# Kernel optimization log

Measured on AMD Instinct MI355X. Metric: run time of the kernel, lower is better.

Reference implementation:

```python
import jax, jax.numpy as jnp
import numpy as np

B = 4
T, Hh, Ww = 16, 32, 32
C = 256
HEADS = 8
WIN = 4
SHIFT = 2
MLP = 1024


def _rel_pos_index(w):
    coords = np.stack(np.meshgrid(np.arange(w), np.arange(w), np.arange(w), indexing='ij')).reshape(3, -1)
    rc = (coords[:, :, None] - coords[:, None, :]).transpose(1, 2, 0)
    rc[:, :, 0] += w - 1
    rc[:, :, 1] += w - 1
    rc[:, :, 2] += w - 1
    rc[:, :, 0] *= (2 * w - 1) * (2 * w - 1)
    rc[:, :, 1] *= 2 * w - 1
    return rc.sum(-1).astype(np.int32)  # (w^3, w^3)


def _attn_mask(t, h, w, win, shift):
    m = np.zeros((t, h, w))
    sl = (slice(0, -win), slice(-win, -shift), slice(-shift, None))
    cnt = 0
    for a in sl:
        for b in sl:
            for c in sl:
                m[a, b, c] = cnt
                cnt += 1
    m = m.reshape(t // win, win, h // win, win, w // win, win).transpose(0, 2, 4, 1, 3, 5).reshape(-1, win ** 3)
    am = m[:, None, :] - m[:, :, None]  # (nW, N, N)
    return np.where(am != 0, -100.0, 0.0).astype(np.float32)


def setup_inputs() -> dict:
    key = jax.random.key(0)
    ks = jax.random.split(key, 12)
    s_in = 1.0 / np.sqrt(C)
    s_mlp = 1.0 / np.sqrt(MLP)
    return {
        'x': jax.random.normal(ks[0], (B, T * Hh * Ww, C), jnp.float32),
        'norm1_g': jnp.ones((C,), jnp.float32),
        'norm1_b': jnp.zeros((C,), jnp.float32),
        'qkv_w': jax.random.normal(ks[1], (C, 3 * C), jnp.float32) * s_in,
        'qkv_b': jax.random.normal(ks[2], (3 * C,), jnp.float32) * 0.02,
        'proj_w': jax.random.normal(ks[3], (C, C), jnp.float32) * s_in,
        'proj_b': jax.random.normal(ks[4], (C,), jnp.float32) * 0.02,
        'rel_bias_table': jax.random.normal(ks[5], ((2 * WIN - 1) ** 3, HEADS), jnp.float32) * 0.02,
        'norm2_g': jnp.ones((C,), jnp.float32),
        'norm2_b': jnp.zeros((C,), jnp.float32),
        'mlp_w1': jax.random.normal(ks[6], (C, MLP), jnp.float32) * s_in,
        'mlp_b1': jax.random.normal(ks[7], (MLP,), jnp.float32) * 0.02,
        'mlp_w2': jax.random.normal(ks[8], (MLP, C), jnp.float32) * s_mlp,
        'mlp_b2': jax.random.normal(ks[9], (C,), jnp.float32) * 0.02,
        'rel_index': jnp.asarray(_rel_pos_index(WIN)),
        'attn_mask': jnp.asarray(_attn_mask(T, Hh, Ww, WIN, SHIFT)),
    }


def _ln(x, g, b, eps):
    mu = x.mean(-1, keepdims=True)
    var = ((x - mu) ** 2).mean(-1, keepdims=True)
    return (x - mu) * jax.lax.rsqrt(var + eps) * g + b


def reference(x, norm1_g, norm1_b, qkv_w, qkv_b, proj_w, proj_b, rel_bias_table,
              norm2_g, norm2_b, mlp_w1, mlp_b1, mlp_w2, mlp_b2, rel_index, attn_mask):
    w = WIN
    N = w ** 3
    hd = C // HEADS
    scale = hd ** -0.5

    h = _ln(x, norm1_g, norm1_b, 1e-5).reshape(B, T, Hh, Ww, C)
    h = jnp.roll(h, shift=(-SHIFT, -SHIFT, -SHIFT), axis=(1, 2, 3))
    # window partition -> (B*nW, N, C)
    h = h.reshape(B, T // w, w, Hh // w, w, Ww // w, w, C)
    h = h.transpose(0, 1, 3, 5, 2, 4, 6, 7).reshape(-1, N, C)

    qkv = (h @ qkv_w + qkv_b).reshape(-1, N, 3, HEADS, hd)
    qkv = qkv.transpose(2, 0, 3, 1, 4)  # (3, BW, heads, N, hd)
    q, k, v = qkv[0] * scale, qkv[1], qkv[2]
    attn = jnp.einsum('bhid,bhjd->bhij', q, k)

    bias = rel_bias_table[rel_index.reshape(-1)].reshape(N, N, HEADS).transpose(2, 0, 1)
    attn = attn + bias[None]

    nW = attn_mask.shape[0]
    attn = attn.reshape(-1, nW, HEADS, N, N) + attn_mask[None, :, None]
    attn = jax.nn.softmax(attn.reshape(-1, HEADS, N, N), axis=-1)

    o = jnp.einsum('bhij,bhjd->bhid', attn, v).transpose(0, 2, 1, 3).reshape(-1, N, C)
    o = o @ proj_w + proj_b
    # window reverse
    o = o.reshape(B, T // w, Hh // w, Ww // w, w, w, w, C)
    o = o.transpose(0, 1, 4, 2, 5, 3, 6, 7).reshape(B, T, Hh, Ww, C)
    o = jnp.roll(o, shift=(SHIFT, SHIFT, SHIFT), axis=(1, 2, 3)).reshape(B, T * Hh * Ww, C)

    x = x + o
    y = _ln(x, norm2_g, norm2_b, 1e-6)
    y = jax.nn.gelu(y @ mlp_w1 + mlp_b1, approximate=False) @ mlp_w2 + mlp_b2
    return x + y
```

## Files before the change

### kernel.cpp

```cpp
#include <hip/hip_runtime.h>
#include <cstdint>
#include <cstddef>

typedef float  f32x4_t  __attribute__((ext_vector_type(4)));
typedef __bf16 bf16x8_t __attribute__((ext_vector_type(8)));
typedef __bf16 bf16x4_t __attribute__((ext_vector_type(4)));

#define NTOK   65536
#define CCH    256
#define NWINT  1024

__device__ __forceinline__ float wred_sum(float v) {
#pragma unroll
  for (int off = 32; off > 0; off >>= 1) v += __shfl_xor(v, off, 64);
  return v;
}

__device__ __forceinline__ void gload16(void* lds, const void* g) {
  __builtin_amdgcn_global_load_lds(
      (const __attribute__((address_space(1))) uint32_t*)g,
      (__attribute__((address_space(3))) uint32_t*)lds, 16, 0, 0);
}

__device__ __forceinline__ int win_to_orig(int token) {
  int gid = token >> 6, n = token & 63;
  int bb = gid >> 8, rem = gid & 255;
  int t = (((rem >> 6) << 2) + (n >> 4) + 2) & 15;
  int h = ((((rem >> 3) & 7) << 2) + ((n >> 2) & 3) + 2) & 31;
  int w = (((rem & 7) << 2) + (n & 3) + 2) & 31;
  return ((bb * 16 + t) * 32 + h) * 32 + w;
}

__global__ __launch_bounds__(256) void prep_weights(
    const float* __restrict__ qkv_w, const float* __restrict__ proj_w,
    const float* __restrict__ mlp_w1, const float* __restrict__ mlp_w2,
    __bf16* __restrict__ wt_qkv, __bf16* __restrict__ wt_proj,
    __bf16* __restrict__ wt_mlp1, __bf16* __restrict__ wt_mlp2) {
  int i = blockIdx.x * 256 + threadIdx.x;
  if (i < 196608) {
    int k = i / 768, n = i % 768;
    wt_qkv[n * 256 + k] = (__bf16)qkv_w[i];
  } else if (i < 262144) {
    int j = i - 196608;
    int k = j >> 8, n = j & 255;
    wt_proj[n * 256 + k] = (__bf16)proj_w[j];
  } else if (i < 524288) {
    int j = i - 262144;
    int k = j >> 10, n = j & 1023;
    wt_mlp1[n * 256 + k] = (__bf16)mlp_w1[j];
  } else {
    int j = i - 524288;
    int k = j >> 8, n = j & 255;
    wt_mlp2[n * 1024 + k] = (__bf16)mlp_w2[j];
  }
}

__global__ __launch_bounds__(256) void cm_prep(
    const float* __restrict__ table, const int* __restrict__ ridx,
    const float* __restrict__ mask, __bf16* __restrict__ cm) {
  int tid = blockIdx.x * 256 + threadIdx.x;
  int l = tid & 63;
  int t16 = (tid >> 6) & 15;
  int h = (tid >> 10) & 7;
  int w = tid >> 13;
  int it = t16 & 3, jt = t16 >> 2;
  int i = it * 16 + (l & 15);
  int jb = jt * 16 + ((l >> 4) << 2);
  const float* mrow = mask + (size_t)w * 4096 + i * 64;
  const int* rrow = ridx + i * 64;
  bf16x4_t o;
#pragma unroll
  for (int r = 0; r < 4; ++r) {
    int j = jb + r;
    o[r] = (__bf16)(table[rrow[j] * 8 + h] + mrow[j]);
  }
  *(bf16x4_t*)(cm + (size_t)tid * 4) = o;
}

template <int MODE>
__global__ __launch_bounds__(256) void ln_kernel(
    const float* __restrict__ xin, const float* __restrict__ g,
    const float* __restrict__ b, __bf16* __restrict__ out, float eps) {
  int token = blockIdx.x * 4 + (threadIdx.x >> 6);
  int lane = threadIdx.x & 63;
  size_t src = (MODE == 0) ? (size_t)win_to_orig(token) : (size_t)token;
  f32x4_t v = ((const f32x4_t*)(xin + src * CCH))[lane];
  float mu = wred_sum(v[0] + v[1] + v[2] + v[3]) * (1.0f / 256.0f);
  float d0 = v[0] - mu, d1 = v[1] - mu, d2 = v[2] - mu, d3 = v[3] - mu;
  float var = wred_sum(d0 * d0 + d1 * d1 + d2 * d2 + d3 * d3) * (1.0f / 256.0f);
  float rs = rsqrtf(var + eps);
  f32x4_t gg = ((const f32x4_t*)g)[lane];
  f32x4_t bb = ((const f32x4_t*)b)[lane];
  bf16x4_t o;
  o[0] = (__bf16)(d0 * rs * gg[0] + bb[0]);
  o[1] = (__bf16)(d1 * rs * gg[1] + bb[1]);
  o[2] = (__bf16)(d2 * rs * gg[2] + bb[2]);
  o[3] = (__bf16)(d3 * rs * gg[3] + bb[3]);
  *(bf16x4_t*)(out + (size_t)token * CCH + lane * 4) = o;
}

#define BM 128
#define BN 128
#define BK 64
template <int EPI>
__global__ __launch_bounds__(256) void gemm_kernel(
    const __bf16* __restrict__ A, const __bf16* __restrict__ Bt,
    const float* __restrict__ bias, const float* __restrict__ res,
    void* __restrict__ outp, int M, int N, int K) {
  __shared__ __bf16 smA[2][8192];
  __shared__ __bf16 smB[2][8192];
  const int wv = threadIdx.x >> 6;
  const int ln = threadIdx.x & 63;
  const int i15 = ln & 15, g = ln >> 4;

  int nwg = gridDim.x;
  int wgid = ((int)blockIdx.x & 7) * (nwg >> 3) + ((int)blockIdx.x >> 3);
  int nx = N >> 7;
  int bx = wgid % nx, by = wgid / nx;
  const int bm = by * BM, bn = bx * BN;
  const int wr = wv >> 1, wc = wv & 1;

  const __bf16* aP[4];
  const __bf16* bP[4];
#pragma unroll
  for (int it = 0; it < 4; ++it) {
    int slot = (it * 4 + wv) * 64 + ln;
    int row = slot >> 3;
    int chunk = (slot & 7) ^ (row & 7);
    aP[it] = A + (size_t)(bm + row) * K + chunk * 8;
    bP[it] = Bt + (size_t)(bn + row) * K + chunk * 8;
  }

  f32x4_t acc[4][4];
#pragma unroll
  for (int m = 0; m < 4; ++m)
#pragma unroll
    for (int n = 0; n < 4; ++n) acc[m][n] = (f32x4_t){0.f, 0.f, 0.f, 0.f};

  const int KT = K >> 6;

  auto stage = [&](int buf) {
#pragma unroll
    for (int it = 0; it < 4; ++it) {
      int base = (it * 4 + wv) * 512;
      gload16(&smA[buf][base], aP[it]);
      gload16(&smB[buf][base], bP[it]);
      aP[it] += BK;
      bP[it] += BK;
    }
  };

  auto compute = [&](int buf) {
    const __bf16* lA = smA[buf];
    const __bf16* lB = smB[buf];
#pragma unroll
    for (int kh = 0; kh < 2; ++kh) {
      int cA = (((kh * 4) + g) ^ (i15 & 7)) * 8;
      bf16x8_t af[4], bfr[4];
#pragma unroll
      for (int m = 0; m < 4; ++m)
        af[m] = *(const bf16x8_t*)(lA + (wr * 64 + m * 16 + i15) * 64 + cA);
#pragma unroll
      for (int n = 0; n < 4; ++n)
        bfr[n] = *(const bf16x8_t*)(lB + (wc * 64 + n * 16 + i15) * 64 + cA);
#pragma unroll
      for (int m = 0; m < 4; ++m)
#pragma unroll
        for (int n = 0; n < 4; ++n)
          acc[m][n] = __builtin_amdgcn_mfma_f32_16x16x32_bf16(
              af[m], bfr[n], acc[m][n], 0, 0, 0);
    }
  };

  stage(0);
  for (int kt = 0; kt < KT - 1; ++kt) {
    stage((kt + 1) & 1);
    asm volatile("s_waitcnt vmcnt(8)" ::: "memory");
    __builtin_amdgcn_s_barrier();
    asm volatile("" ::: "memory");
    compute(kt & 1);
    asm volatile("s_waitcnt lgkmcnt(0)" ::: "memory");
    __builtin_amdgcn_s_barrier();
  }
  asm volatile("s_waitcnt vmcnt(0)" ::: "memory");
  __builtin_amdgcn_s_barrier();
  asm volatile("" ::: "memory");
  compute((KT - 1) & 1);

  float bv[4];
#pragma unroll
  for (int n = 0; n < 4; ++n) bv[n] = bias[bn + wc * 64 + n * 16 + i15];
#pragma unroll
  for (int m = 0; m < 4; ++m) {
    int grow0 = bm + wr * 64 + m * 16 + g * 4;
#pragma unroll
    for (int r = 0; r < 4; ++r) {
      int grow = grow0 + r;
      size_t rowbase;
      if constexpr (EPI == 1)
        rowbase = (size_t)win_to_orig(grow) * CCH;
      else
        rowbase = (size_t)grow * N;
#pragma unroll
      for (int n = 0; n < 4; ++n) {
        int gcol = bn + wc * 64 + n * 16 + i15;
        float v = acc[m][n][r] + bv[n];
        if constexpr (EPI == 0) {
          ((__bf16*)outp)[rowbase + gcol] = (__bf16)v;
        } else if constexpr (EPI == 1) {
          size_t dst = rowbase + gcol;
          ((float*)outp)[dst] = res[dst] + v;
        } else if constexpr (EPI == 2) {
          float gl = 0.5f * v * (1.0f + erff(v * 0.70710678118654752f));
          ((__bf16*)outp)[rowbase + gcol] = (__bf16)gl;
        } else {
          size_t o = rowbase + gcol;
          ((float*)outp)[o] = res[o] + v;
        }
      }
    }
  }
}

__global__ __launch_bounds__(256) void attn_mfma(
    const __bf16* __restrict__ qkv, const __bf16* __restrict__ cm,
    __bf16* __restrict__ owin) {
  __shared__ __align__(16) __bf16 smP[4][64 * 72];
  __shared__ __align__(16) __bf16 smV[4][64 * 32];
  const int wv = threadIdx.x >> 6;
  const int ln = threadIdx.x & 63;
  const int task = blockIdx.x * 4 + wv;
  const int win = task >> 3;
  const int h = task & 7;
  const int i15 = ln & 15, g = ln >> 4;

  const __bf16* base = qkv + (size_t)win * 64 * 768 + h * 32;

  {
    __bf16* vdst = smV[wv];
#pragma unroll
    for (int c = 0; c < 4; ++c) {
      const __bf16* src =
          base + (size_t)(c * 16 + (ln >> 2)) * 768 + 512 + (ln & 3) * 8;
      gload16(vdst + c * 512, src);
    }
  }

  bf16x8_t kf[4], qf[4];
#pragma unroll
  for (int t = 0; t < 4; ++t) {
    kf[t] = *(const bf16x8_t*)(base + (size_t)(t * 16 + i15) * 768 + 256 + g * 8);
    qf[t] = *(const bf16x8_t*)(base + (size_t)(t * 16 + i15) * 768 + g * 8);
  }

  f32x4_t st[4][4];
#pragma unroll
  for (int jt = 0; jt < 4; ++jt)
#pragma unroll
    for (int it = 0; it < 4; ++it)
      st[jt][it] = __builtin_amdgcn_mfma_f32_16x16x32_bf16(
          kf[jt], qf[it], (f32x4_t){0.f, 0.f, 0.f, 0.f}, 0, 0, 0);

  const __bf16* cmp = cm + (((size_t)(win & 255) * 8 + h) * 16) * 256;
#pragma unroll
  for (int jt = 0; jt < 4; ++jt)
#pragma unroll
    for (int it = 0; it < 4; ++it) {
      bf16x4_t c4 = *(const bf16x4_t*)(cmp + ((jt * 4 + it) * 64 + ln) * 4);
#pragma unroll
      for (int r = 0; r < 4; ++r)
        st[jt][it][r] =
            fmaf(st[jt][it][r], 0.17677669529663687f, (float)c4[r]);
    }

#pragma unroll
  for (int it = 0; it < 4; ++it) {
    float mx = -1e30f;
#pragma unroll
    for (int jt = 0; jt < 4; ++jt)
#pragma unroll
      for (int r = 0; r < 4; ++r) mx = fmaxf(mx, st[jt][it][r]);
    mx = fmaxf(mx, __shfl_xor(mx, 16, 64));
    mx = fmaxf(mx, __shfl_xor(mx, 32, 64));
    float sum = 0.f;
#pragma unroll
    for (int jt = 0; jt < 4; ++jt)
#pragma unroll
      for (int r = 0; r < 4; ++r) {
        float p = __expf(st[jt][it][r] - mx);
        st[jt][it][r] = p;
        sum += p;
      }
    sum += __shfl_xor(sum, 16, 64);
    sum += __shfl_xor(sum, 32, 64);
    float inv = 1.0f / sum;
#pragma unroll
    for (int jt = 0; jt < 4; ++jt) {
      bf16x4_t p4;
#pragma unroll
      for (int r = 0; r < 4; ++r) p4[r] = (__bf16)(st[jt][it][r] * inv);
      *(bf16x4_t*)(smP[wv] + (it * 16 + i15) * 72 + jt * 16 + g * 4) = p4;
    }
  }
  __syncthreads();

  f32x4_t oacc[4][2];
#pragma unroll
  for (int it = 0; it < 4; ++it)
#pragma unroll
    for (int dt = 0; dt < 2; ++dt) oacc[it][dt] = (f32x4_t){0.f, 0.f, 0.f, 0.f};

  const __bf16* pl = smP[wv];
  const __bf16* vl = smV[wv];
#pragma unroll
  for (int kt = 0; kt < 2; ++kt) {
    bf16x8_t vf[2];
#pragma unroll
    for (int dt = 0; dt < 2; ++dt)
#pragma unroll
      for (int e = 0; e < 8; ++e)
        vf[dt][e] = vl[(kt * 32 + g * 8 + e) * 32 + dt * 16 + i15];
#pragma unroll
    for (int it = 0; it < 4; ++it) {
      bf16x8_t pa =
          *(const bf16x8_t*)(pl + (it * 16 + i15) * 72 + kt * 32 + g * 8);
#pragma unroll
      for (int dt = 0; dt < 2; ++dt)
        oacc[it][dt] = __builtin_amdgcn_mfma_f32_16x16x32_bf16(
            pa, vf[dt], oacc[it][dt], 0, 0, 0);
    }
  }

  __bf16* op = owin + (size_t)win * 64 * 256 + h * 32;
#pragma unroll
  for (int it = 0; it < 4; ++it)
#pragma unroll
    for (int r = 0; r < 4; ++r) {
      int i = it * 16 + g * 4 + r;
#pragma unroll
      for (int dt = 0; dt < 2; ++dt)
        op[(size_t)i * 256 + dt * 16 + i15] = (__bf16)oacc[it][dt][r];
    }
}

extern "C" void kernel_launch(void* const* d_in, const int* in_sizes, int n_in,
                              void* d_out, int out_size, void* d_ws,
                              size_t ws_size, hipStream_t stream) {
  (void)in_sizes; (void)n_in; (void)out_size; (void)ws_size;
  const float* x      = (const float*)d_in[0];
  const float* n1g    = (const float*)d_in[1];
  const float* n1b    = (const float*)d_in[2];
  const float* qkv_w  = (const float*)d_in[3];
  const float* qkv_b  = (const float*)d_in[4];
  const float* proj_w = (const float*)d_in[5];
  const float* proj_b = (const float*)d_in[6];
  const float* rbt    = (const float*)d_in[7];
  const float* n2g    = (const float*)d_in[8];
  const float* n2b    = (const float*)d_in[9];
  const float* mlp_w1 = (const float*)d_in[10];
  const float* mlp_b1 = (const float*)d_in[11];
  const float* mlp_w2 = (const float*)d_in[12];
  const float* mlp_b2 = (const float*)d_in[13];
  const int*   ridx   = (const int*)d_in[14];
  const float* amask  = (const float*)d_in[15];

  char* ws = (char*)d_ws;
  size_t off = 0;
  auto alloc = [&](size_t bytes) {
    void* p = ws + off;
    off += (bytes + 255) & ~(size_t)255;
    return p;
  };
  __bf16* wt_qkv  = (__bf16*)alloc(768 * 256 * 2);
  __bf16* wt_proj = (__bf16*)alloc(256 * 256 * 2);
  __bf16* wt_mlp1 = (__bf16*)alloc(1024 * 256 * 2);
  __bf16* wt_mlp2 = (__bf16*)alloc(1024 * 256 * 2);
  __bf16* hwin = (__bf16*)alloc((size_t)NTOK * 256 * 2);
  __bf16* qkv  = (__bf16*)alloc((size_t)NTOK * 768 * 2);
  __bf16* owin = (__bf16*)alloc((size_t)NTOK * 256 * 2);
  __bf16* cmb  = hwin;
  __bf16* yb   = hwin;
  __bf16* mlph = qkv;
  float* x2    = (float*)d_out;

  prep_weights<<<3072, 256, 0, stream>>>(qkv_w, proj_w, mlp_w1, mlp_w2,
                                         wt_qkv, wt_proj, wt_mlp1, wt_mlp2);
  ln_kernel<0><<<NTOK / 4, 256, 0, stream>>>(x, n1g, n1b, hwin, 1e-5f);
  gemm_kernel<0><<<(768 / BN) * (NTOK / BM), 256, 0, stream>>>(
      hwin, wt_qkv, qkv_b, nullptr, qkv, NTOK, 768, 256);
  cm_prep<<<8192, 256, 0, stream>>>(rbt, ridx, amask, cmb);
  attn_mfma<<<2048, 256, 0, stream>>>(qkv, cmb, owin);
  gemm_kernel<1><<<(256 / BN) * (NTOK / BM), 256, 0, stream>>>(
      owin, wt_proj, proj_b, x, x2, NTOK, 256, 256);
  ln_kernel<1><<<NTOK / 4, 256, 0, stream>>>(x2, n2g, n2b, yb, 1e-6f);
  gemm_kernel<2><<<(1024 / BN) * (NTOK / BM), 256, 0, stream>>>(
      yb, wt_mlp1, mlp_b1, nullptr, mlph, NTOK, 1024, 256);
  gemm_kernel<3><<<(256 / BN) * (NTOK / BM), 256, 0, stream>>>(
      mlph, wt_mlp2, mlp_b2, x2, d_out, NTOK, 256, 1024);
}
```

Measured before the change: 359.8 us.

## Widen GEMM tiles to 128x256 with 512 threads and use tanh-GELU

The GEMM kernel moves from 128x128 tiles with 4 waves and double-buffered LDS to 128x256 tiles with 8 waves and a single LDS buffer. It now waits for all loads with a full barrier each K step and relies on higher occupancy (launch bounds 512,4) instead of explicit overlap. The intent is more data reuse per block and better latency hiding across waves, but dropping the prefetch pipeline may expose global-load latency. The exact erf GELU in the MLP epilogue is also replaced by a tanh/exp approximation, trading a small accuracy loss for cheaper math.

```diff
diff --git a/kernel.cpp b/kernel.cpp
--- a/kernel.cpp
+++ b/kernel.cpp
@@ -99,35 +99,41 @@
   *(bf16x4_t*)(out + (size_t)token * CCH + lane * 4) = o;
 }
 
-#define BM 128
-#define BN 128
-#define BK 64
+#define BMG 128
+#define BNG 256
+#define BKG 64
 template <int EPI>
-__global__ __launch_bounds__(256) void gemm_kernel(
+__global__ __launch_bounds__(512, 4) void gemm_kernel(
     const __bf16* __restrict__ A, const __bf16* __restrict__ Bt,
     const float* __restrict__ bias, const float* __restrict__ res,
     void* __restrict__ outp, int M, int N, int K) {
-  __shared__ __bf16 smA[2][8192];
-  __shared__ __bf16 smB[2][8192];
+  __shared__ __bf16 smA[BMG * BKG];
+  __shared__ __bf16 smB[BNG * BKG];
   const int wv = threadIdx.x >> 6;
   const int ln = threadIdx.x & 63;
   const int i15 = ln & 15, g = ln >> 4;
 
   int nwg = gridDim.x;
   int wgid = ((int)blockIdx.x & 7) * (nwg >> 3) + ((int)blockIdx.x >> 3);
-  int nx = N >> 7;
+  int nx = N >> 8;
   int bx = wgid % nx, by = wgid / nx;
-  const int bm = by * BM, bn = bx * BN;
-  const int wr = wv >> 1, wc = wv & 1;
-
-  const __bf16* aP[4];
+  const int bm = by * BMG, bn = bx * BNG;
+  const int wr = wv >> 2, wc = wv & 3;
+
+  const __bf16* aP[2];
   const __bf16* bP[4];
 #pragma unroll
-  for (int it = 0; it < 4; ++it) {
-    int slot = (it * 4 + wv) * 64 + ln;
+  for (int it = 0; it < 2; ++it) {
+    int slot = (it * 8 + wv) * 64 + ln;
     int row = slot >> 3;
     int chunk = (slot & 7) ^ (row & 7);
     aP[it] = A + (size_t)(bm + row) * K + chunk * 8;
+  }
+#pragma unroll
+  for (int it = 0; it < 4; ++it) {
+    int slot = (it * 8 + wv) * 64 + ln;
+    int row = slot >> 3;
+    int chunk = (slot & 7) ^ (row & 7);
     bP[it] = Bt + (size_t)(bn + row) * K + chunk * 8;
   }
 
@@ -138,31 +144,30 @@
     for (int n = 0; n < 4; ++n) acc[m][n] = (f32x4_t){0.f, 0.f, 0.f, 0.f};
 
   const int KT = K >> 6;
-
-  auto stage = [&](int buf) {
+  for (int kt = 0; kt < KT; ++kt) {
+#pragma unroll
+    for (int it = 0; it < 2; ++it) {
+      gload16(&smA[(it * 8 + wv) * 512], aP[it]);
+      aP[it] += BKG;
+    }
 #pragma unroll
     for (int it = 0; it < 4; ++it) {
-      int base = (it * 4 + wv) * 512;
-      gload16(&smA[buf][base], aP[it]);
-      gload16(&smB[buf][base], bP[it]);
-      aP[it] += BK;
-      bP[it] += BK;
-    }
-  };
-
-  auto compute = [&](int buf) {
-    const __bf16* lA = smA[buf];
-    const __bf16* lB = smB[buf];
+      gload16(&smB[(it * 8 + wv) * 512], bP[it]);
+      bP[it] += BKG;
+    }
+    asm volatile("s_waitcnt vmcnt(0)" ::: "memory");
+    __syncthreads();
+
 #pragma unroll
     for (int kh = 0; kh < 2; ++kh) {
-      int cA = (((kh * 4) + g) ^ (i15 & 7)) * 8;
+      int co = ((kh * 4 + g) ^ (i15 & 7)) * 8;
       bf16x8_t af[4], bfr[4];
 #pragma unroll
       for (int m = 0; m < 4; ++m)
-        af[m] = *(const bf16x8_t*)(lA + (wr * 64 + m * 16 + i15) * 64 + cA);
+        af[m] = *(const bf16x8_t*)(smA + (wr * 64 + m * 16 + i15) * 64 + co);
 #pragma unroll
       for (int n = 0; n < 4; ++n)
-        bfr[n] = *(const bf16x8_t*)(lB + (wc * 64 + n * 16 + i15) * 64 + cA);
+        bfr[n] = *(const bf16x8_t*)(smB + (wc * 64 + n * 16 + i15) * 64 + co);
 #pragma unroll
       for (int m = 0; m < 4; ++m)
 #pragma unroll
@@ -170,22 +175,8 @@
           acc[m][n] = __builtin_amdgcn_mfma_f32_16x16x32_bf16(
               af[m], bfr[n], acc[m][n], 0, 0, 0);
     }
-  };
-
-  stage(0);
-  for (int kt = 0; kt < KT - 1; ++kt) {
-    stage((kt + 1) & 1);
-    asm volatile("s_waitcnt vmcnt(8)" ::: "memory");
-    __builtin_amdgcn_s_barrier();
-    asm volatile("" ::: "memory");
-    compute(kt & 1);
-    asm volatile("s_waitcnt lgkmcnt(0)" ::: "memory");
-    __builtin_amdgcn_s_barrier();
-  }
-  asm volatile("s_waitcnt vmcnt(0)" ::: "memory");
-  __builtin_amdgcn_s_barrier();
-  asm volatile("" ::: "memory");
-  compute((KT - 1) & 1);
+    __syncthreads();
+  }
 
   float bv[4];
 #pragma unroll
@@ -211,7 +202,9 @@
           size_t dst = rowbase + gcol;
           ((float*)outp)[dst] = res[dst] + v;
         } else if constexpr (EPI == 2) {
-          float gl = 0.5f * v * (1.0f + erff(v * 0.70710678118654752f));
+          float u = v * (0.7978845608028654f + 0.03567740814f * v * v);
+          float t = 1.0f - 2.0f / (__expf(2.0f * u) + 1.0f);
+          float gl = 0.5f * v * (1.0f + t);
           ((__bf16*)outp)[rowbase + gcol] = (__bf16)gl;
         } else {
           size_t o = rowbase + gcol;
@@ -386,15 +379,15 @@
   prep_weights<<<3072, 256, 0, stream>>>(qkv_w, proj_w, mlp_w1, mlp_w2,
                                          wt_qkv, wt_proj, wt_mlp1, wt_mlp2);
   ln_kernel<0><<<NTOK / 4, 256, 0, stream>>>(x, n1g, n1b, hwin, 1e-5f);
-  gemm_kernel<0><<<(768 / BN) * (NTOK / BM), 256, 0, stream>>>(
+  gemm_kernel<0><<<(768 / BNG) * (NTOK / BMG), 512, 0, stream>>>(
       hwin, wt_qkv, qkv_b, nullptr, qkv, NTOK, 768, 256);
   cm_prep<<<8192, 256, 0, stream>>>(rbt, ridx, amask, cmb);
   attn_mfma<<<2048, 256, 0, stream>>>(qkv, cmb, owin);
-  gemm_kernel<1><<<(256 / BN) * (NTOK / BM), 256, 0, stream>>>(
+  gemm_kernel<1><<<(256 / BNG) * (NTOK / BMG), 512, 0, stream>>>(
       owin, wt_proj, proj_b, x, x2, NTOK, 256, 256);
   ln_kernel<1><<<NTOK / 4, 256, 0, stream>>>(x2, n2g, n2b, yb, 1e-6f);
-  gemm_kernel<2><<<(1024 / BN) * (NTOK / BM), 256, 0, stream>>>(
+  gemm_kernel<2><<<(1024 / BNG) * (NTOK / BMG), 512, 0, stream>>>(
       yb, wt_mlp1, mlp_b1, nullptr, mlph, NTOK, 1024, 256);
-  gemm_kernel<3><<<(256 / BN) * (NTOK / BM), 256, 0, stream>>>(
+  gemm_kernel<3><<<(256 / BNG) * (NTOK / BMG), 512, 0, stream>>>(
       mlph, wt_mlp2, mlp_b2, x2, d_out, NTOK, 256, 1024);
 }
```

New measurement: 303.6 us. 15.6% less time.
